# Kernel optimization log

Measured on AMD Instinct MI355X. Metric: run time of the kernel, lower is better.

Reference implementation:

```python
import jax, jax.numpy as jnp
import numpy as np

B, S, HID = 1, 2048, 2048
H, NOPE, ROPE, VDIM = 16, 128, 64, 128
QR, KVR = 1536, 512
IH, ID = 16, 128
TOPK = 512
THETA = 10000.0
EPS = 1e-6
SCALE = (NOPE + ROPE) ** -0.5
NEG = -1e9


def _cos_sin(s, dim, dtype):
    inv = 1.0 / (THETA ** (np.arange(0, dim, 2, dtype=np.float32) / dim))
    t = np.arange(s, dtype=np.float32)
    f = np.outer(t, inv)
    emb = np.concatenate([f, f], -1)
    return jnp.asarray(np.cos(emb), dtype), jnp.asarray(np.sin(emb), dtype)


def _rope(x, cos, sin):
    # x: [b,s,h,d]; cos/sin: [s,d]; NeoX-style rotate_half
    x1, x2 = jnp.split(x, 2, axis=-1)
    rot = jnp.concatenate([-x2, x1], axis=-1)
    return x * cos[None, :, None, :] + rot * sin[None, :, None, :]


def _rmsnorm(x, w):
    v = jnp.mean(x.astype(jnp.float32) ** 2, -1, keepdims=True)
    return (x.astype(jnp.float32) * jax.lax.rsqrt(v + EPS)).astype(x.dtype) * w


def _layernorm(x, w, b):
    m = jnp.mean(x, -1, keepdims=True)
    v = jnp.var(x, -1, keepdims=True)
    return (x - m) * jax.lax.rsqrt(v + EPS) * w + b


def setup_inputs() -> dict:
    key = jax.random.key(0)
    ks = jax.random.split(key, 12)
    g = lambda k, shp: jax.random.normal(k, shp, jnp.float32) * 0.02
    return {
        'hidden_states': jax.random.normal(ks[0], (B, S, HID), jnp.float32),
        'q_a_w': g(ks[1], (QR, HID)),
        'q_a_ln_w': jnp.ones((QR,), jnp.float32),
        'q_b_w': g(ks[2], (H * (NOPE + ROPE), QR)),
        'kv_a_w': g(ks[3], (KVR + ROPE, HID)),
        'kv_a_ln_w': jnp.ones((KVR,), jnp.float32),
        'kv_b_w': g(ks[4], (H * (NOPE + VDIM), KVR)),
        'o_w': g(ks[5], (HID, H * VDIM)),
        'idx_wq_b_w': g(ks[6], (IH * ID, QR)),
        'idx_wk_w': g(ks[7], (ID, HID)),
        'idx_kn_w': jnp.ones((ID,), jnp.float32),
        'idx_kn_b': jnp.zeros((ID,), jnp.float32),
        'idx_wproj_w': g(ks[8], (IH, HID)),
    }


def reference(hidden_states, q_a_w, q_a_ln_w, q_b_w, kv_a_w, kv_a_ln_w, kv_b_w, o_w,
              idx_wq_b_w, idx_wk_w, idx_kn_w, idx_kn_b, idx_wproj_w):
    b, s, _ = hidden_states.shape
    cos, sin = _cos_sin(s, ROPE, hidden_states.dtype)

    # --- MLA projections ---
    qr = _rmsnorm(hidden_states @ q_a_w.T, q_a_ln_w)                 # [b,s,QR]
    q = (qr @ q_b_w.T).reshape(b, s, H, NOPE + ROPE)
    q_nope, q_pe = q[..., :NOPE], q[..., NOPE:]
    q_pe = _rope(q_pe, cos, sin)
    ckv = hidden_states @ kv_a_w.T                                   # [b,s,KVR+ROPE]
    c_kv, k_pe = ckv[..., :KVR], ckv[..., KVR:]
    k_pe = _rope(k_pe[:, :, None, :], cos, sin)                      # [b,s,1,ROPE]
    kv = (_rmsnorm(c_kv, kv_a_ln_w) @ kv_b_w.T).reshape(b, s, H, NOPE + VDIM)
    k_nope, v = kv[..., :NOPE], kv[..., NOPE:]

    # --- DSA indexer: per-token importance scores ---
    iq = (qr @ idx_wq_b_w.T).reshape(b, s, IH, ID)
    iq = jnp.concatenate([_rope(iq[..., :ROPE], cos, sin), iq[..., ROPE:]], -1)
    ik = _layernorm(hidden_states @ idx_wk_w.T, idx_kn_w, idx_kn_b)  # [b,s,ID]
    ik_pe = _rope(ik[:, :, None, :ROPE], cos, sin)[:, :, 0, :]
    ik = jnp.concatenate([ik_pe, ik[..., ROPE:]], -1)
    iw = (hidden_states @ idx_wproj_w.T) * (IH ** -0.5)              # [b,s,IH]
    idx_scores = jnp.einsum('bqh,bhqk->bqk', iw,
                            jax.nn.relu(jnp.einsum('bqhd,bkd->bhqk', iq, ik)))
    causal = jnp.tril(jnp.ones((s, s), bool))
    idx_scores = jnp.where(causal[None], idx_scores, -jnp.inf)
    _, top_idx = jax.lax.top_k(idx_scores, TOPK)                     # [b,s,TOPK]
    bi = jnp.arange(b)[:, None, None]
    qi = jnp.arange(s)[None, :, None]
    keep = jnp.zeros((b, s, s), bool).at[bi, qi, top_idx].set(True)
    allowed = keep & causal[None]                                    # [b,s,s]

    # --- sparse top-k attention (top-k mask to -inf before softmax) ---
    qh = jnp.concatenate([q_nope, q_pe], -1)                         # [b,s,H,192]
    kh = jnp.concatenate([k_nope, jnp.broadcast_to(k_pe, (b, s, H, ROPE))], -1)
    scores = jnp.einsum('bqhd,bkhd->bhqk', qh, kh) * SCALE
    scores = jnp.where(allowed[:, None], scores, NEG)
    attn = jax.nn.softmax(scores, -1)
    out = jnp.einsum('bhqk,bkhd->bqhd', attn, v).reshape(b, s, H * VDIM)
    return out @ o_w.T
```

## Files before the change

### kernel.cpp

```cpp
#include <hip/hip_runtime.h>
#include <hip/hip_bf16.h>
#include <math.h>

#define SEQ 2048
#define HIDD 2048
#define QRANK 1536
#define KVRANK 512
#define TOPK 512
#define EPSF 1e-6f
#define SCALE_ATTN 0.07216878364870323f
#define NCAT 1680

typedef __attribute__((ext_vector_type(8))) short short8v;
typedef __attribute__((ext_vector_type(4))) short short4v;
typedef __attribute__((ext_vector_type(4))) float f32x4;

__device__ inline unsigned short f2bf(float f) {
    unsigned u = __float_as_uint(f);
    unsigned r = (u + 0x7FFFu + ((u >> 16) & 1u)) >> 16;
    return (unsigned short)r;
}
__device__ inline float bf2f(unsigned short b) {
    return __uint_as_float(((unsigned)b) << 16);
}
__device__ inline void split2(float x, unsigned short& h, unsigned short& l) {
    h = f2bf(x);
    l = f2bf(x - bf2f(h));
}

__device__ inline short4v ds_read_tr16(const void* p) {
#if __has_builtin(__builtin_amdgcn_ds_read_tr16_b64)
    return __builtin_amdgcn_ds_read_tr16_b64((short4v*)p);
#else
    const unsigned short* u = (const unsigned short*)p;
    short4v r;
    r[0] = (short)u[0]; r[1] = (short)u[16]; r[2] = (short)u[32]; r[3] = (short)u[48];
    return r;
#endif
}

__global__ void rope_table_kernel(float* __restrict__ cos_t, float* __restrict__ sin_t) {
    int s = blockIdx.x;
    int i = threadIdx.x;
    double inv = pow(10000.0, -((double)(2 * i)) / 64.0);
    double f = (double)s * inv;
    cos_t[s * 32 + i] = (float)cos(f);
    sin_t[s * 32 + i] = (float)sin(f);
}

__global__ __launch_bounds__(256) void cvt_bf16_kernel(const float* __restrict__ in,
                                                       unsigned short* __restrict__ out, int n4) {
    for (int i = blockIdx.x * 256 + threadIdx.x; i < n4; i += gridDim.x * 256) {
        float4 v = ((const float4*)in)[i];
        ushort4 o;
        o.x = f2bf(v.x); o.y = f2bf(v.y); o.z = f2bf(v.z); o.w = f2bf(v.w);
        ((ushort4*)out)[i] = o;
    }
}

__global__ __launch_bounds__(256) void wkt_kernel(const float* __restrict__ kvb,
                                                  unsigned short* __restrict__ wkt) {
    __shared__ float t[128][129];
    int h = blockIdx.x, n0 = blockIdx.y * 128;
    int tid = threadIdx.x;
    for (int it = tid; it < 128 * 32; it += 256) {
        int d = it >> 5, c4 = it & 31;
        float4 v = *(const float4*)(kvb + ((size_t)(h * 256 + d)) * 512 + n0 + c4 * 4);
        t[d][c4 * 4 + 0] = v.x; t[d][c4 * 4 + 1] = v.y;
        t[d][c4 * 4 + 2] = v.z; t[d][c4 * 4 + 3] = v.w;
    }
    __syncthreads();
    for (int it = tid; it < 128 * 32; it += 256) {
        int n = it >> 5, dc = it & 31;
        ushort4 o;
        o.x = f2bf(t[dc * 4 + 0][n]); o.y = f2bf(t[dc * 4 + 1][n]);
        o.z = f2bf(t[dc * 4 + 2][n]); o.w = f2bf(t[dc * 4 + 3][n]);
        *(ushort4*)(wkt + ((size_t)h * 512 + n0 + n) * 128 + dc * 4) = o;
    }
}

__global__ __launch_bounds__(256) void gemm_cat_split_kernel(
    const float* __restrict__ hidden, const float* __restrict__ q_a_w,
    const float* __restrict__ idx_wk_w, const float* __restrict__ idx_wproj_w,
    float* __restrict__ ccat)
{
    __shared__ __align__(16) unsigned short Ah[128 * 32], Al[128 * 32];
    __shared__ __align__(16) unsigned short Bh[128 * 32], Bl[128 * 32];
    int tid = threadIdx.x;
    int l = tid & 63, w = tid >> 6;
    int wr = w >> 1, wc = w & 1;
    int m0 = blockIdx.x * 128, n0 = blockIdx.y * 128;
    f32x4 acc[4][4] = {};
    for (int k0 = 0; k0 < HIDD; k0 += 32) {
        __syncthreads();
#pragma unroll
        for (int i = 0; i < 2; ++i) {
            int idx = tid + i * 256;
            int r = idx >> 2, cc = idx & 3;
            int sw = cc ^ (r & 3);
            {
                const float* src = hidden + (size_t)(m0 + r) * HIDD + k0 + cc * 8;
                float4 f0 = *(const float4*)src, f1 = *(const float4*)(src + 4);
                float xs[8] = {f0.x, f0.y, f0.z, f0.w, f1.x, f1.y, f1.z, f1.w};
                short8v dh, dl;
#pragma unroll
                for (int e = 0; e < 8; ++e) {
                    unsigned short hh, ll; split2(xs[e], hh, ll);
                    dh[e] = (short)hh; dl[e] = (short)ll;
                }
                *(short8v*)&Ah[r * 32 + sw * 8] = dh;
                *(short8v*)&Al[r * 32 + sw * 8] = dl;
            }
            {
                int gb = n0 + r; if (gb > NCAT - 1) gb = NCAT - 1;
                float scale = 1.f;
                const float* src;
                if (gb < 1536) src = q_a_w + (size_t)gb * HIDD;
                else if (gb < 1664) src = idx_wk_w + (size_t)(gb - 1536) * HIDD;
                else { src = idx_wproj_w + (size_t)(gb - 1664) * HIDD; scale = 0.25f; }
                src += k0 + cc * 8;
                float4 f0 = *(const float4*)src, f1 = *(const float4*)(src + 4);
                float xs[8] = {f0.x, f0.y, f0.z, f0.w, f1.x, f1.y, f1.z, f1.w};
                short8v dh, dl;
#pragma unroll
                for (int e = 0; e < 8; ++e) {
                    unsigned short hh, ll; split2(xs[e] * scale, hh, ll);
                    dh[e] = (short)hh; dl[e] = (short)ll;
                }
                *(short8v*)&Bh[r * 32 + sw * 8] = dh;
                *(short8v*)&Bl[r * 32 + sw * 8] = dl;
            }
        }
        __syncthreads();
        short8v avh[4], avl[4];
#pragma unroll
        for (int mt = 0; mt < 4; ++mt) {
            int row = wr * 64 + mt * 16 + (l & 15);
            int ch = (l >> 4) ^ (row & 3);
            avh[mt] = *(const short8v*)&Ah[row * 32 + ch * 8];
            avl[mt] = *(const short8v*)&Al[row * 32 + ch * 8];
        }
#pragma unroll
        for (int nt = 0; nt < 4; ++nt) {
            int row = wc * 64 + nt * 16 + (l & 15);
            int ch = (l >> 4) ^ (row & 3);
            short8v bvh = *(const short8v*)&Bh[row * 32 + ch * 8];
            short8v bvl = *(const short8v*)&Bl[row * 32 + ch * 8];
#pragma unroll
            for (int mt = 0; mt < 4; ++mt) {
                acc[mt][nt] = __builtin_amdgcn_mfma_f32_16x16x32_bf16(avh[mt], bvh, acc[mt][nt], 0, 0, 0);
                acc[mt][nt] = __builtin_amdgcn_mfma_f32_16x16x32_bf16(avh[mt], bvl, acc[mt][nt], 0, 0, 0);
                acc[mt][nt] = __builtin_amdgcn_mfma_f32_16x16x32_bf16(avl[mt], bvh, acc[mt][nt], 0, 0, 0);
            }
        }
    }
#pragma unroll
    for (int mt = 0; mt < 4; ++mt)
#pragma unroll
        for (int nt = 0; nt < 4; ++nt)
#pragma unroll
            for (int i = 0; i < 4; ++i) {
                int gm = m0 + wr * 64 + mt * 16 + (l >> 4) * 4 + i;
                int gn = n0 + wc * 64 + nt * 16 + (l & 15);
                if (gn < NCAT) ccat[(size_t)gm * NCAT + gn] = acc[mt][nt][i];
            }
}

__global__ __launch_bounds__(256) void gemm_iq_split_kernel(
    const float* __restrict__ qr, const float* __restrict__ wq,
    const float* __restrict__ cos_t, const float* __restrict__ sin_t,
    unsigned short* __restrict__ iqh, unsigned short* __restrict__ iql)
{
    __shared__ __align__(16) unsigned short Ah[128 * 32], Al[128 * 32];
    __shared__ __align__(16) unsigned short Bh[128 * 32], Bl[128 * 32];
    int tid = threadIdx.x;
    int l = tid & 63, w = tid >> 6;
    int wr = w >> 1, wc = w & 1;
    int m0 = blockIdx.x * 128, n0 = blockIdx.y * 128;
    int hh_ = blockIdx.y;
    f32x4 acc[4][4] = {};
    for (int k0 = 0; k0 < QRANK; k0 += 32) {
        __syncthreads();
#pragma unroll
        for (int i = 0; i < 2; ++i) {
            int idx = tid + i * 256;
            int r = idx >> 2, cc = idx & 3;
            int sw = cc ^ (r & 3);
            {
                const float* src = qr + (size_t)(m0 + r) * QRANK + k0 + cc * 8;
                float4 f0 = *(const float4*)src, f1 = *(const float4*)(src + 4);
                float xs[8] = {f0.x, f0.y, f0.z, f0.w, f1.x, f1.y, f1.z, f1.w};
                short8v dh, dl;
#pragma unroll
                for (int e = 0; e < 8; ++e) {
                    unsigned short h2, l2; split2(xs[e], h2, l2);
                    dh[e] = (short)h2; dl[e] = (short)l2;
                }
                *(short8v*)&Ah[r * 32 + sw * 8] = dh;
                *(short8v*)&Al[r * 32 + sw * 8] = dl;
            }
            {
                const float* src = wq + (size_t)(n0 + r) * QRANK + k0 + cc * 8;
                float4 f0 = *(const float4*)src, f1 = *(const float4*)(src + 4);
                float xs[8] = {f0.x, f0.y, f0.z, f0.w, f1.x, f1.y, f1.z, f1.w};
                short8v dh, dl;
#pragma unroll
                for (int e = 0; e < 8; ++e) {
                    unsigned short h2, l2; split2(xs[e], h2, l2);
                    dh[e] = (short)h2; dl[e] = (short)l2;
                }
                *(short8v*)&Bh[r * 32 + sw * 8] = dh;
                *(short8v*)&Bl[r * 32 + sw * 8] = dl;
            }
        }
        __syncthreads();
        short8v avh[4], avl[4];
#pragma unroll
        for (int mt = 0; mt < 4; ++mt) {
            int row = wr * 64 + mt * 16 + (l & 15);
            int ch = (l >> 4) ^ (row & 3);
            avh[mt] = *(const short8v*)&Ah[row * 32 + ch * 8];
            avl[mt] = *(const short8v*)&Al[row * 32 + ch * 8];
        }
#pragma unroll
        for (int nt = 0; nt < 4; ++nt) {
            int row = wc * 64 + nt * 16 + (l & 15);
            int ch = (l >> 4) ^ (row & 3);
            short8v bvh = *(const short8v*)&Bh[row * 32 + ch * 8];
            short8v bvl = *(const short8v*)&Bl[row * 32 + ch * 8];
#pragma unroll
            for (int mt = 0; mt < 4; ++mt) {
                acc[mt][nt] = __builtin_amdgcn_mfma_f32_16x16x32_bf16(avh[mt], bvh, acc[mt][nt], 0, 0, 0);
                acc[mt][nt] = __builtin_amdgcn_mfma_f32_16x16x32_bf16(avh[mt], bvl, acc[mt][nt], 0, 0, 0);
                acc[mt][nt] = __builtin_amdgcn_mfma_f32_16x16x32_bf16(avl[mt], bvh, acc[mt][nt], 0, 0, 0);
            }
        }
    }
    if (wc == 0) {
#pragma unroll
        for (int mt = 0; mt < 4; ++mt)
#pragma unroll
            for (int nt = 0; nt < 2; ++nt)
#pragma unroll
                for (int i = 0; i < 4; ++i) {
                    int q = m0 + wr * 64 + mt * 16 + (l >> 4) * 4 + i;
                    int dd = nt * 16 + (l & 15);
                    float c = cos_t[q * 32 + dd], s = sin_t[q * 32 + dd];
                    float x1 = acc[mt][nt][i], x2 = acc[mt][nt + 2][i];
                    acc[mt][nt][i] = x1 * c - x2 * s;
                    acc[mt][nt + 2][i] = x2 * c + x1 * s;
                }
    }
#pragma unroll
    for (int mt = 0; mt < 4; ++mt)
#pragma unroll
        for (int nt = 0; nt < 4; ++nt)
#pragma unroll
            for (int i = 0; i < 4; ++i) {
                int q = m0 + wr * 64 + mt * 16 + (l >> 4) * 4 + i;
                int d = wc * 64 + nt * 16 + (l & 15);
                size_t idx = ((size_t)q * 16 + hh_) * 128 + d;
                unsigned short h2, l2; split2(acc[mt][nt][i], h2, l2);
                iqh[idx] = h2; iql[idx] = l2;
            }
}

template <typename TA, typename TC>
__global__ __launch_bounds__(256) void mfma_nt_kernel(
    const TA* __restrict__ A, const unsigned short* __restrict__ B, TC* __restrict__ C,
    int M, int N, int K, int lda, int ldb, int ldc, long ab, long bb, long cb,
    const float* __restrict__ cos_t, const float* __restrict__ sin_t, int rope_mode)
{
    __shared__ __align__(16) unsigned short Asl[128 * 32];
    __shared__ __align__(16) unsigned short Bsl[128 * 32];
    int z = blockIdx.z;
    const TA* Az = A + (size_t)z * ab;
    const unsigned short* Bz = B + (size_t)z * bb;
    TC* Cz = C + (size_t)z * cb;
    int tid = threadIdx.x;
    int l = tid & 63, w = tid >> 6;
    int wr = w >> 1, wc = w & 1;
    int m0 = blockIdx.x * 128, n0 = blockIdx.y * 128;
    f32x4 acc[4][4] = {};

    for (int k0 = 0; k0 < K; k0 += 32) {
        __syncthreads();
#pragma unroll
        for (int i = 0; i < 2; ++i) {
            int idx = tid + i * 256;
            int r = idx >> 2, cc = idx & 3;
            int sw = cc ^ (r & 3);
            {
                short8v d;
                const TA* src = Az + (size_t)(m0 + r) * lda + k0 + cc * 8;
                if constexpr (sizeof(TA) == 2) {
                    d = *(const short8v*)src;
                } else {
                    float4 f0 = *(const float4*)src;
                    float4 f1 = *(const float4*)(src + 4);
                    d[0] = (short)f2bf(f0.x); d[1] = (short)f2bf(f0.y);
                    d[2] = (short)f2bf(f0.z); d[3] = (short)f2bf(f0.w);
                    d[4] = (short)f2bf(f1.x); d[5] = (short)f2bf(f1.y);
                    d[6] = (short)f2bf(f1.z); d[7] = (short)f2bf(f1.w);
                }
                *(short8v*)&Asl[r * 32 + sw * 8] = d;
            }
            {
                int gb = n0 + r; if (gb > N - 1) gb = N - 1;
                short8v d = *(const short8v*)(Bz + (size_t)gb * ldb + k0 + cc * 8);
                *(short8v*)&Bsl[r * 32 + sw * 8] = d;
            }
        }
        __syncthreads();
        short8v av[4], bv[4];
#pragma unroll
        for (int mt = 0; mt < 4; ++mt) {
            int row = wr * 64 + mt * 16 + (l & 15);
            int ch = (l >> 4) ^ (row & 3);
            av[mt] = *(const short8v*)&Asl[row * 32 + ch * 8];
        }
#pragma unroll
        for (int nt = 0; nt < 4; ++nt) {
            int row = wc * 64 + nt * 16 + (l & 15);
            int ch = (l >> 4) ^ (row & 3);
            bv[nt] = *(const short8v*)&Bsl[row * 32 + ch * 8];
        }
#pragma unroll
        for (int mt = 0; mt < 4; ++mt)
#pragma unroll
            for (int nt = 0; nt < 4; ++nt)
                acc[mt][nt] = __builtin_amdgcn_mfma_f32_16x16x32_bf16(av[mt], bv[nt], acc[mt][nt], 0, 0, 0);
    }
    if (rope_mode) {
        int gcol64 = (n0 >> 6) + wc;
        bool dorope = (rope_mode == 1) ? ((gcol64 % 3) == 2) : (gcol64 == 8);
        if (dorope) {
#pragma unroll
            for (int mt = 0; mt < 4; ++mt)
#pragma unroll
                for (int nt = 0; nt < 2; ++nt)
#pragma unroll
                    for (int i = 0; i < 4; ++i) {
                        int q = m0 + wr * 64 + mt * 16 + (l >> 4) * 4 + i;
                        int dd = nt * 16 + (l & 15);
                        float c = cos_t[q * 32 + dd], sn = sin_t[q * 32 + dd];
                        float x1 = acc[mt][nt][i], x2 = acc[mt][nt + 2][i];
                        acc[mt][nt][i] = x1 * c - x2 * sn;
                        acc[mt][nt + 2][i] = x2 * c + x1 * sn;
                    }
        }
    }
#pragma unroll
    for (int mt = 0; mt < 4; ++mt) {
#pragma unroll
        for (int nt = 0; nt < 4; ++nt) {
#pragma unroll
            for (int i = 0; i < 4; ++i) {
                int gm = m0 + wr * 64 + mt * 16 + (l >> 4) * 4 + i;
                int gn = n0 + wc * 64 + nt * 16 + (l & 15);
                if (gn < N) {
                    float v = acc[mt][nt][i];
                    if constexpr (sizeof(TC) == 4) Cz[(size_t)gm * ldc + gn] = v;
                    else Cz[(size_t)gm * ldc + gn] = f2bf(v);
                }
            }
        }
    }
}

__global__ __launch_bounds__(256) void rmsnorm_kernel(
    const float* __restrict__ in, const float* __restrict__ w, float* __restrict__ out,
    unsigned short* __restrict__ bf_out, int n, int in_stride)
{
    int row = blockIdx.x, tid = threadIdx.x;
    const float* x = in + (size_t)row * in_stride;
    float4 v[2];
    int cnt = 0;
    float ss = 0.f;
    int nf4 = n >> 2;
    for (int i = tid; i < nf4; i += 256) {
        float4 t = *(const float4*)(x + i * 4);
        v[cnt++] = t;
        ss += t.x * t.x + t.y * t.y + t.z * t.z + t.w * t.w;
    }
#pragma unroll
    for (int m = 32; m; m >>= 1) ss += __shfl_xor(ss, m);
    __shared__ float red[8];
    int wid = tid >> 6;
    if ((tid & 63) == 0) red[wid] = ss;
    __syncthreads();
    if (tid == 0) {
        float s = red[0] + red[1] + red[2] + red[3];
        red[4] = rsqrtf(s / (float)n + EPSF);
    }
    __syncthreads();
    float scale = red[4];
    cnt = 0;
    for (int i = tid; i < nf4; i += 256) {
        float4 t = v[cnt++];
        float4 wv = *(const float4*)(w + i * 4);
        float4 o;
        o.x = t.x * scale * wv.x; o.y = t.y * scale * wv.y;
        o.z = t.z * scale * wv.z; o.w = t.w * scale * wv.w;
        *(float4*)(out + (size_t)row * n + i * 4) = o;
        if (bf_out) {
            ushort4 ob;
            ob.x = f2bf(o.x); ob.y = f2bf(o.y); ob.z = f2bf(o.z); ob.w = f2bf(o.w);
            *(ushort4*)(bf_out + (size_t)row * n + i * 4) = ob;
        }
    }
}

__global__ __launch_bounds__(256) void rmsnorm_khg_kernel(
    const float* __restrict__ ckv, const float* __restrict__ w,
    unsigned short* __restrict__ khg)
{
    int row = blockIdx.x, tid = threadIdx.x;
    const float* x = ckv + (size_t)row * 576;
    float4 v = make_float4(0.f, 0.f, 0.f, 0.f);
    float ss = 0.f;
    if (tid < 128) {
        v = *(const float4*)(x + tid * 4);
        ss = v.x * v.x + v.y * v.y + v.z * v.z + v.w * v.w;
    }
#pragma unroll
    for (int mm = 32; mm; mm >>= 1) ss += __shfl_xor(ss, mm);
    __shared__ float red[8];
    if ((tid & 63) == 0) red[tid >> 6] = ss;
    __syncthreads();
    if (tid == 0) red[4] = rsqrtf((red[0] + red[1] + red[2] + red[3]) * (1.f / 512.f) + EPSF);
    __syncthreads();
    float scale = red[4];
    if (tid < 128) {
        float4 wv = *(const float4*)(w + tid * 4);
        ushort4 ob;
        ob.x = f2bf(v.x * scale * wv.x); ob.y = f2bf(v.y * scale * wv.y);
        ob.z = f2bf(v.z * scale * wv.z); ob.w = f2bf(v.w * scale * wv.w);
        *(ushort4*)(khg + (size_t)row * 576 + tid * 4) = ob;
    } else if (tid < 192) {
        khg[(size_t)row * 576 + 512 + (tid - 128)] = f2bf(x[512 + tid - 128]);
    }
}

__global__ __launch_bounds__(64) void ln_rope_split_kernel(
    const float* __restrict__ in, int stride,
    const float* __restrict__ w, const float* __restrict__ b,
    const float* __restrict__ cos_t, const float* __restrict__ sin_t,
    unsigned short* __restrict__ ikh, unsigned short* __restrict__ ikl)
{
    int row = blockIdx.x, tid = threadIdx.x;
    const float* x = in + (size_t)row * stride;
    float x0 = x[tid], x1 = x[tid + 64];
    float s = x0 + x1, ss = x0 * x0 + x1 * x1;
#pragma unroll
    for (int m = 32; m; m >>= 1) { s += __shfl_xor(s, m); ss += __shfl_xor(ss, m); }
    float mean = s * (1.f / 128.f);
    float var = ss * (1.f / 128.f) - mean * mean;
    float r = rsqrtf(var + EPSF);
    float n0 = (x0 - mean) * r * w[tid] + b[tid];
    float n1 = (x1 - mean) * r * w[tid + 64] + b[tid + 64];
    float c = cos_t[row * 32 + (tid & 31)], sn = sin_t[row * 32 + (tid & 31)];
    float other = __shfl_xor(n0, 32);
    float r0 = (tid < 32) ? (n0 * c - other * sn) : (n0 * c + other * sn);
    unsigned short h2, l2;
    split2(r0, h2, l2);
    ikh[(size_t)row * 128 + tid] = h2; ikl[(size_t)row * 128 + tid] = l2;
    split2(n1, h2, l2);
    ikh[(size_t)row * 128 + 64 + tid] = h2; ikl[(size_t)row * 128 + 64 + tid] = l2;
}

__global__ __launch_bounds__(256) void idx_scores_mfma_kernel(
    const unsigned short* __restrict__ iqh, const unsigned short* __restrict__ iql,
    const unsigned short* __restrict__ ikh, const unsigned short* __restrict__ ikl,
    const float* __restrict__ iwsrc, int iw_stride,
    float* __restrict__ scores)
{
    int q0 = blockIdx.x * 64, k0 = blockIdx.y * 64;
    int tid = threadIdx.x;
    if (k0 > q0 + 63) {
        for (int t = tid; t < 64 * 64; t += 256) {
            int r = t >> 6, c = t & 63;
            scores[(size_t)(q0 + r) * SEQ + k0 + c] = -INFINITY;
        }
        return;
    }
    __shared__ __align__(16) unsigned short skh[64 * 128], skl[64 * 128];
    __shared__ __align__(16) unsigned short sqh[64 * 128], sql[64 * 128];
    __shared__ float iws[64][16];
    int l = tid & 63, w = tid >> 6;
    for (int it = tid; it < 64 * 16; it += 256) {
        int r = it >> 4, c = it & 15;
        int sw = c ^ (r & 15);
        *(short8v*)&skh[r * 128 + sw * 8] = *(const short8v*)(ikh + (size_t)(k0 + r) * 128 + c * 8);
        *(short8v*)&skl[r * 128 + sw * 8] = *(const short8v*)(ikl + (size_t)(k0 + r) * 128 + c * 8);
    }
    {
        int r = tid >> 2, c = tid & 3;
        *(float4*)&iws[r][c * 4] = *(const float4*)(iwsrc + (size_t)(q0 + r) * iw_stride + c * 4);
    }
    f32x4 acc[4] = {};
    for (int h = 0; h < 16; ++h) {
        __syncthreads();
        for (int it = tid; it < 64 * 16; it += 256) {
            int r = it >> 4, c = it & 15;
            int sw = c ^ (r & 15);
            size_t base = ((size_t)(q0 + r) * 16 + h) * 128 + c * 8;
            *(short8v*)&sqh[r * 128 + sw * 8] = *(const short8v*)(iqh + base);
            *(short8v*)&sql[r * 128 + sw * 8] = *(const short8v*)(iql + base);
        }
        __syncthreads();
        f32x4 dot[4] = {};
#pragma unroll
        for (int ks = 0; ks < 4; ++ks) {
            int arow = w * 16 + (l & 15);
            int ach = ((l >> 4) + ks * 4) ^ (arow & 15);
            short8v ah = *(const short8v*)&sqh[arow * 128 + ach * 8];
            short8v al = *(const short8v*)&sql[arow * 128 + ach * 8];
#pragma unroll
            for (int nt = 0; nt < 4; ++nt) {
                int brow = nt * 16 + (l & 15);
                int bch = ((l >> 4) + ks * 4) ^ (brow & 15);
                short8v bh = *(const short8v*)&skh[brow * 128 + bch * 8];
                short8v bl = *(const short8v*)&skl[brow * 128 + bch * 8];
                dot[nt] = __builtin_amdgcn_mfma_f32_16x16x32_bf16(ah, bh, dot[nt], 0, 0, 0);
                dot[nt] = __builtin_amdgcn_mfma_f32_16x16x32_bf16(ah, bl, dot[nt], 0, 0, 0);
                dot[nt] = __builtin_amdgcn_mfma_f32_16x16x32_bf16(al, bh, dot[nt], 0, 0, 0);
            }
        }
#pragma unroll
        for (int nt = 0; nt < 4; ++nt)
#pragma unroll
            for (int i = 0; i < 4; ++i) {
                float wv = iws[w * 16 + (l >> 4) * 4 + i][h];
                acc[nt][i] += wv * fmaxf(dot[nt][i], 0.f);
            }
    }
#pragma unroll
    for (int nt = 0; nt < 4; ++nt)
#pragma unroll
        for (int i = 0; i < 4; ++i) {
            int q = q0 + w * 16 + (l >> 4) * 4 + i;
            int k = k0 + nt * 16 + (l & 15);
            scores[(size_t)q * SEQ + k] = (k <= q) ? acc[nt][i] : -INFINITY;
        }
}

__global__ __launch_bounds__(1024) void topk_kernel(
    const float* __restrict__ scores, int* __restrict__ sel)
{
    int qi = blockIdx.x, tid = threadIdx.x;
    __shared__ unsigned long long keys[2048];
    const float* srow = scores + (size_t)qi * SEQ;
#pragma unroll
    for (int r = 0; r < 2; ++r) {
        int k = tid + r * 1024;
        unsigned u = __float_as_uint(srow[k]);
        unsigned mv = (u & 0x80000000u) ? ~u : (u | 0x80000000u);
        keys[k] = ((unsigned long long)mv << 32) | (unsigned)(2047 - k);
    }
    for (int ksz = 2; ksz <= 2048; ksz <<= 1) {
        for (int j = ksz >> 1; j > 0; j >>= 1) {
            __syncthreads();
#pragma unroll 1
            for (int r = 0; r < 2; ++r) {
                int i = tid + r * 1024;
                int ixj = i ^ j;
                if (ixj > i) {
                    unsigned long long a = keys[i], b = keys[ixj];
                    bool dir = ((i & ksz) == 0);
                    if ((a < b) == dir) { keys[i] = b; keys[ixj] = a; }
                }
            }
        }
    }
    __syncthreads();
    if (tid < TOPK) {
        int k = 2047 - (int)(keys[tid] & 0xFFFFFFFFu);
        sel[(size_t)qi * TOPK + tid] = (tid <= qi) ? k : -1;
    }
}

__global__ __launch_bounds__(256) void attn_mfma_kernel(
    const unsigned short* __restrict__ qabs,
    const float* __restrict__ qsrc,
    const unsigned short* __restrict__ khg,
    const int* __restrict__ sel,
    unsigned short* __restrict__ ocomp)
{
    __shared__ __align__(16) char smem[39424];
    unsigned short* plds = (unsigned short*)(smem + 38016);
    float* smax = (float*)(smem + 39040);
    float* ssum = (float*)(smem + 39168);
    int* selb   = (int*)(smem + 39296);

    const int qi = blockIdx.x;
    const int tid = threadIdx.x;
    const int l = tid & 63, w = tid >> 6;
    const int lg = l >> 4, lr = l & 15;
    const int nv = min(TOPK, qi + 1);
    const int ntile = (nv + 31) >> 5;
    const int krow = w * 16 + lr;

    short8v aq[18];
    {
        const unsigned short* qa = qabs + ((size_t)qi * 16 + lr) * 512 + lg * 8;
#pragma unroll
        for (int ks = 0; ks < 16; ++ks)
            aq[ks] = *(const short8v*)(qa + ks * 32);
        const float* qp = qsrc + (size_t)qi * 3072 + lr * 192 + 128 + lg * 8;
#pragma unroll
        for (int ks = 0; ks < 2; ++ks) {
            float4 f0 = *(const float4*)(qp + ks * 32);
            float4 f1 = *(const float4*)(qp + ks * 32 + 4);
            short8v d;
            d[0] = (short)f2bf(f0.x); d[1] = (short)f2bf(f0.y);
            d[2] = (short)f2bf(f0.z); d[3] = (short)f2bf(f0.w);
            d[4] = (short)f2bf(f1.x); d[5] = (short)f2bf(f1.y);
            d[6] = (short)f2bf(f1.z); d[7] = (short)f2bf(f1.w);
            aq[16 + ks] = d;
        }
    }

    const int sbase = krow * 32 + (lg >> 1) * 1056 + (lg & 1) * 16;
    const int vboff = w * 8 * 1056 + lg * 256 + lr * 2;

    float m[4] = {-1e30f, -1e30f, -1e30f, -1e30f};
    float lsum[4] = {0.f, 0.f, 0.f, 0.f};
    f32x4 oacc[8] = {};

    for (int t = 0; t < ntile; ++t) {
        const int j0 = t * 32;
        __syncthreads();
        if (tid < 32) {
            int sv = sel[(size_t)qi * TOPK + j0 + tid];
            selb[tid] = sv < 0 ? 0 : sv;
        }
        __syncthreads();
        for (int it = tid; it < 32 * 64; it += 256) {
            int key = it >> 6, c = it & 63;
            short8v v = *(const short8v*)(khg + (size_t)selb[key] * 576 + c * 8);
            *(short8v*)(smem + (c >> 1) * 1056 + key * 32 + (c & 1) * 16) = v;
        }
        {
            int key = tid >> 3, c = tid & 7;
            short8v v = *(const short8v*)(khg + (size_t)selb[key] * 576 + 512 + c * 8);
            *(short8v*)(smem + (32 + (c >> 1)) * 1056 + key * 32 + (c & 1) * 16) = v;
        }
        __syncthreads();
        f32x4 s = {};
        if (w < 2) {
            __builtin_amdgcn_s_setprio(1);
#pragma unroll
            for (int ks = 0; ks < 18; ++ks) {
                short8v b = *(const short8v*)(smem + sbase + ks * 2112);
                s = __builtin_amdgcn_mfma_f32_16x16x32_bf16(aq[ks], b, s, 0, 0, 0);
            }
            __builtin_amdgcn_s_setprio(0);
            bool kvalid = (j0 + krow) < nv;
#pragma unroll
            for (int i = 0; i < 4; ++i)
                s[i] = kvalid ? s[i] * SCALE_ATTN : -1e30f;
            float tm[4];
#pragma unroll
            for (int i = 0; i < 4; ++i) tm[i] = s[i];
#pragma unroll
            for (int sh = 1; sh < 16; sh <<= 1)
#pragma unroll
                for (int i = 0; i < 4; ++i) tm[i] = fmaxf(tm[i], __shfl_xor(tm[i], sh));
            if (lr == 0) *(float4*)&smax[w * 16 + lg * 4] = make_float4(tm[0], tm[1], tm[2], tm[3]);
        }
        __syncthreads();
        float mn[4], scl[4];
#pragma unroll
        for (int i = 0; i < 4; ++i) {
            int h = lg * 4 + i;
            float tmax = fmaxf(smax[h], smax[16 + h]);
            mn[i] = fmaxf(m[i], tmax);
            scl[i] = __expf(m[i] - mn[i]);
            m[i] = mn[i];
        }
        if (w < 2) {
            float p[4], rs[4];
#pragma unroll
            for (int i = 0; i < 4; ++i) { p[i] = __expf(s[i] - mn[i]); rs[i] = p[i]; }
#pragma unroll
            for (int sh = 1; sh < 16; sh <<= 1)
#pragma unroll
                for (int i = 0; i < 4; ++i) rs[i] += __shfl_xor(rs[i], sh);
            if (lr == 0) *(float4*)&ssum[w * 16 + lg * 4] = make_float4(rs[0], rs[1], rs[2], rs[3]);
            ushort4 pb;
            pb.x = f2bf(p[0]); pb.y = f2bf(p[1]); pb.z = f2bf(p[2]); pb.w = f2bf(p[3]);
            *(ushort4*)&plds[krow * 16 + lg * 4] = pb;
        }
        __syncthreads();
#pragma unroll
        for (int i = 0; i < 4; ++i) {
            int h = lg * 4 + i;
            lsum[i] = lsum[i] * scl[i] + (ssum[h] + ssum[16 + h]);
        }
#pragma unroll
        for (int nt = 0; nt < 8; ++nt)
#pragma unroll
            for (int i = 0; i < 4; ++i) oacc[nt][i] *= scl[i];
        short8v af;
#pragma unroll
        for (int j = 0; j < 8; ++j)
            af[j] = (short)plds[(lg * 8 + j) * 16 + lr];
        __builtin_amdgcn_s_setprio(1);
#pragma unroll
        for (int nt = 0; nt < 8; ++nt) {
            const char* a = smem + vboff + nt * 1056;
            short4v t0 = ds_read_tr16(a);
            short4v t1 = ds_read_tr16(a + 128);
            short8v bf = __builtin_shufflevector(t0, t1, 0, 1, 2, 3, 4, 5, 6, 7);
            oacc[nt] = __builtin_amdgcn_mfma_f32_16x16x32_bf16(af, bf, oacc[nt], 0, 0, 0);
        }
        __builtin_amdgcn_s_setprio(0);
    }
    float inv[4];
#pragma unroll
    for (int i = 0; i < 4; ++i) inv[i] = 1.f / lsum[i];
    unsigned short* ob = ocomp + (size_t)qi * 16 * 512;
#pragma unroll
    for (int nt = 0; nt < 8; ++nt) {
        int d = w * 128 + nt * 16 + lr;
#pragma unroll
        for (int i = 0; i < 4; ++i) {
            int h = lg * 4 + i;
            ob[h * 512 + d] = f2bf(oacc[nt][i] * inv[i]);
        }
    }
}

extern "C" void kernel_launch(void* const* d_in, const int* in_sizes, int n_in,
                              void* d_out, int out_size, void* d_ws, size_t ws_size,
                              hipStream_t stream) {
    (void)in_sizes; (void)n_in; (void)out_size; (void)ws_size;
    const float* hidden      = (const float*)d_in[0];
    const float* q_a_w       = (const float*)d_in[1];
    const float* q_a_ln_w    = (const float*)d_in[2];
    const float* q_b_w       = (const float*)d_in[3];
    const float* kv_a_w      = (const float*)d_in[4];
    const float* kv_a_ln_w   = (const float*)d_in[5];
    const float* kv_b_w      = (const float*)d_in[6];
    const float* o_w         = (const float*)d_in[7];
    const float* idx_wq_b_w  = (const float*)d_in[8];
    const float* idx_wk_w    = (const float*)d_in[9];
    const float* idx_kn_w    = (const float*)d_in[10];
    const float* idx_kn_b    = (const float*)d_in[11];
    const float* idx_wproj_w = (const float*)d_in[12];
    float* out = (float*)d_out;

    char* ws = (char*)d_ws;
    size_t off = 0;
    auto alloc = [&](size_t nbytes) -> void* {
        void* p = ws + off;
        off = (off + nbytes + 255) & ~(size_t)255;
        return p;
    };
    float* cos_t = (float*)alloc((size_t)SEQ * 32 * 4);
    float* sin_t = (float*)alloc((size_t)SEQ * 32 * 4);
    float* qbuf  = (float*)alloc((size_t)SEQ * 3072 * 4);
    float* ckv   = (float*)alloc((size_t)SEQ * 576 * 4);
    int*   sel   = (int*)alloc((size_t)SEQ * TOPK * 4);
    unsigned short* khg      = (unsigned short*)alloc((size_t)SEQ * 576 * 2);
    unsigned short* attno_bf = (unsigned short*)alloc((size_t)SEQ * 2048 * 2);
    unsigned short* qr_bf    = (unsigned short*)alloc((size_t)SEQ * QRANK * 2);
    unsigned short* q_b_bf   = (unsigned short*)alloc((size_t)3072 * QRANK * 2);
    unsigned short* kv_a_bf  = (unsigned short*)alloc((size_t)576 * HIDD * 2);
    unsigned short* o_w_bf   = (unsigned short*)alloc((size_t)HIDD * 2048 * 2);
    unsigned short* kv_b_bf  = (unsigned short*)alloc((size_t)4096 * 512 * 2);
    unsigned short* wkt      = (unsigned short*)alloc((size_t)16 * 512 * 128 * 2);
    size_t mark = off;
    float* qr    = (float*)alloc((size_t)SEQ * QRANK * 4);
    float* ccat  = (float*)alloc((size_t)SEQ * NCAT * 4);
    float* scores = (float*)alloc((size_t)SEQ * SEQ * 4);
    unsigned short* iqh = (unsigned short*)alloc((size_t)SEQ * 2048 * 2);
    unsigned short* iql = (unsigned short*)alloc((size_t)SEQ * 2048 * 2);
    unsigned short* ikh = (unsigned short*)alloc((size_t)SEQ * 128 * 2);
    unsigned short* ikl = (unsigned short*)alloc((size_t)SEQ * 128 * 2);
    off = mark;
    unsigned short* qabsb = (unsigned short*)alloc((size_t)SEQ * 16 * 512 * 2);
    unsigned short* ocomp = (unsigned short*)alloc((size_t)SEQ * 16 * 512 * 2);

    rope_table_kernel<<<dim3(SEQ), dim3(32), 0, stream>>>(cos_t, sin_t);

    cvt_bf16_kernel<<<1024, 256, 0, stream>>>(q_b_w, q_b_bf, 3072 * QRANK / 4);
    cvt_bf16_kernel<<<1024, 256, 0, stream>>>(kv_a_w, kv_a_bf, 576 * HIDD / 4);
    cvt_bf16_kernel<<<1024, 256, 0, stream>>>(o_w, o_w_bf, HIDD * 2048 / 4);
    cvt_bf16_kernel<<<1024, 256, 0, stream>>>(kv_b_w, kv_b_bf, 4096 * 512 / 4);
    wkt_kernel<<<dim3(16, 4), 256, 0, stream>>>(kv_b_w, wkt);

    gemm_cat_split_kernel<<<dim3(16, 14), 256, 0, stream>>>(hidden, q_a_w, idx_wk_w, idx_wproj_w, ccat);

    rmsnorm_kernel<<<SEQ, 256, 0, stream>>>(ccat, q_a_ln_w, qr, qr_bf, QRANK, NCAT);

    ln_rope_split_kernel<<<SEQ, 64, 0, stream>>>(ccat + 1536, NCAT, idx_kn_w, idx_kn_b, cos_t, sin_t, ikh, ikl);

    mfma_nt_kernel<unsigned short, float><<<dim3(16, 24, 1), 256, 0, stream>>>(
        qr_bf, q_b_bf, qbuf, SEQ, 3072, QRANK, QRANK, QRANK, 3072, 0L, 0L, 0L,
        cos_t, sin_t, 1);

    mfma_nt_kernel<float, float><<<dim3(16, 5, 1), 256, 0, stream>>>(
        hidden, kv_a_bf, ckv, SEQ, 576, HIDD, HIDD, HIDD, 576, 0L, 0L, 0L,
        cos_t, sin_t, 2);
    rmsnorm_khg_kernel<<<SEQ, 256, 0, stream>>>(ckv, kv_a_ln_w, khg);

    gemm_iq_split_kernel<<<dim3(16, 16), 256, 0, stream>>>(qr, idx_wq_b_w, cos_t, sin_t, iqh, iql);

    idx_scores_mfma_kernel<<<dim3(32, 32), 256, 0, stream>>>(iqh, iql, ikh, ikl, ccat + 1664, NCAT, scores);
    topk_kernel<<<SEQ, 1024, 0, stream>>>(scores, sel);

    mfma_nt_kernel<float, unsigned short><<<dim3(16, 4, 16), 256, 0, stream>>>(
        qbuf, wkt, qabsb, SEQ, 512, 128, 3072, 128, 16 * 512,
        192L, 512L * 128L, 512L, nullptr, nullptr, 0);

    attn_mfma_kernel<<<SEQ, 256, 0, stream>>>(qabsb, qbuf, khg, sel, ocomp);

    mfma_nt_kernel<unsigned short, unsigned short><<<dim3(16, 1, 16), 256, 0, stream>>>(
        ocomp, kv_b_bf + (size_t)128 * 512, attno_bf, SEQ, 128, 512,
        16 * 512, 512, 2048, 512L, 256L * 512L, 128L, nullptr, nullptr, 0);

    mfma_nt_kernel<unsigned short, float><<<dim3(16, 16, 1), 256, 0, stream>>>(
        attno_bf, o_w_bf, out, SEQ, HIDD, 2048, 2048, 2048, HIDD, 0L, 0L, 0L,
        nullptr, nullptr, 0);
}
```

Baseline: 960.0 us.

## Widen attention key tiles to 64, hoist indexer K fragments, merge bf16 conversions

The sparse attention kernel now processes 64 selected keys per tile instead of 32, so all four waves compute scores rather than two. The rope part of K moves to a separate XOR-swizzled LDS region, and PV runs as two k-blocks. LDS use roughly doubles, which may lower occupancy. The indexer score kernel loads the K high/low fragments into registers once instead of reloading them from LDS for every head, at the cost of many more VGPRs. The four weight-conversion launches are merged into one kernel to cut launch overhead.

```diff
diff --git a/kernel.cpp b/kernel.cpp
--- a/kernel.cpp
+++ b/kernel.cpp
@@ -48,13 +48,23 @@
     sin_t[s * 32 + i] = (float)sin(f);
 }
 
-__global__ __launch_bounds__(256) void cvt_bf16_kernel(const float* __restrict__ in,
-                                                       unsigned short* __restrict__ out, int n4) {
-    for (int i = blockIdx.x * 256 + threadIdx.x; i < n4; i += gridDim.x * 256) {
-        float4 v = ((const float4*)in)[i];
+__global__ __launch_bounds__(256) void cvt_bf16_4_kernel(
+    const float* __restrict__ a, int na4, const float* __restrict__ b, int nb4,
+    const float* __restrict__ c, int nc4, const float* __restrict__ d, int nd4,
+    unsigned short* __restrict__ oa, unsigned short* __restrict__ ob,
+    unsigned short* __restrict__ oc, unsigned short* __restrict__ od)
+{
+    int total = na4 + nb4 + nc4 + nd4;
+    for (int i = blockIdx.x * 256 + threadIdx.x; i < total; i += gridDim.x * 256) {
+        const float* src; unsigned short* dst; int j = i;
+        if (j < na4) { src = a; dst = oa; }
+        else if ((j -= na4) < nb4) { src = b; dst = ob; }
+        else if ((j -= nb4) < nc4) { src = c; dst = oc; }
+        else { j -= nc4; src = d; dst = od; }
+        float4 v = ((const float4*)src)[j];
         ushort4 o;
         o.x = f2bf(v.x); o.y = f2bf(v.y); o.z = f2bf(v.z); o.w = f2bf(v.w);
-        ((ushort4*)out)[i] = o;
+        ((ushort4*)dst)[j] = o;
     }
 }
 
@@ -498,6 +508,17 @@
         int r = tid >> 2, c = tid & 3;
         *(float4*)&iws[r][c * 4] = *(const float4*)(iwsrc + (size_t)(q0 + r) * iw_stride + c * 4);
     }
+    __syncthreads();
+    short8v bhr[4][4], blr[4][4];
+#pragma unroll
+    for (int nt = 0; nt < 4; ++nt)
+#pragma unroll
+        for (int ks = 0; ks < 4; ++ks) {
+            int brow = nt * 16 + (l & 15);
+            int bch = ((l >> 4) + ks * 4) ^ (brow & 15);
+            bhr[nt][ks] = *(const short8v*)&skh[brow * 128 + bch * 8];
+            blr[nt][ks] = *(const short8v*)&skl[brow * 128 + bch * 8];
+        }
     f32x4 acc[4] = {};
     for (int h = 0; h < 16; ++h) {
         __syncthreads();
@@ -518,13 +539,9 @@
             short8v al = *(const short8v*)&sql[arow * 128 + ach * 8];
 #pragma unroll
             for (int nt = 0; nt < 4; ++nt) {
-                int brow = nt * 16 + (l & 15);
-                int bch = ((l >> 4) + ks * 4) ^ (brow & 15);
-                short8v bh = *(const short8v*)&skh[brow * 128 + bch * 8];
-                short8v bl = *(const short8v*)&skl[brow * 128 + bch * 8];
-                dot[nt] = __builtin_amdgcn_mfma_f32_16x16x32_bf16(ah, bh, dot[nt], 0, 0, 0);
-                dot[nt] = __builtin_amdgcn_mfma_f32_16x16x32_bf16(ah, bl, dot[nt], 0, 0, 0);
-                dot[nt] = __builtin_amdgcn_mfma_f32_16x16x32_bf16(al, bh, dot[nt], 0, 0, 0);
+                dot[nt] = __builtin_amdgcn_mfma_f32_16x16x32_bf16(ah, bhr[nt][ks], dot[nt], 0, 0, 0);
+                dot[nt] = __builtin_amdgcn_mfma_f32_16x16x32_bf16(ah, blr[nt][ks], dot[nt], 0, 0, 0);
+                dot[nt] = __builtin_amdgcn_mfma_f32_16x16x32_bf16(al, bhr[nt][ks], dot[nt], 0, 0, 0);
             }
         }
 #pragma unroll
@@ -587,18 +604,18 @@
     const int* __restrict__ sel,
     unsigned short* __restrict__ ocomp)
 {
-    __shared__ __align__(16) char smem[39424];
-    unsigned short* plds = (unsigned short*)(smem + 38016);
-    float* smax = (float*)(smem + 39040);
-    float* ssum = (float*)(smem + 39168);
-    int* selb   = (int*)(smem + 39296);
+    __shared__ __align__(16) char smem[77568];
+    unsigned short* plds = (unsigned short*)(smem + 74752);
+    float* smax = (float*)(smem + 76800);
+    float* ssum = (float*)(smem + 77056);
+    int* selb   = (int*)(smem + 77312);
 
     const int qi = blockIdx.x;
     const int tid = threadIdx.x;
     const int l = tid & 63, w = tid >> 6;
     const int lg = l >> 4, lr = l & 15;
     const int nv = min(TOPK, qi + 1);
-    const int ntile = (nv + 31) >> 5;
+    const int ntile = (nv + 63) >> 6;
     const int krow = w * 16 + lr;
 
     short8v aq[18];
@@ -621,101 +638,105 @@
         }
     }
 
-    const int sbase = krow * 32 + (lg >> 1) * 1056 + (lg & 1) * 16;
-    const int vboff = w * 8 * 1056 + lg * 256 + lr * 2;
+    const int sbase = krow * 32 + (lg >> 1) * 2080 + (lg & 1) * 16;
+    const int vboff = w * 16640 + lg * 256 + lr * 2;
 
     float m[4] = {-1e30f, -1e30f, -1e30f, -1e30f};
     float lsum[4] = {0.f, 0.f, 0.f, 0.f};
     f32x4 oacc[8] = {};
 
     for (int t = 0; t < ntile; ++t) {
-        const int j0 = t * 32;
-        __syncthreads();
-        if (tid < 32) {
+        const int j0 = t * 64;
+        __syncthreads();
+        if (tid < 64) {
             int sv = sel[(size_t)qi * TOPK + j0 + tid];
             selb[tid] = sv < 0 ? 0 : sv;
         }
         __syncthreads();
-        for (int it = tid; it < 32 * 64; it += 256) {
+        for (int it = tid; it < 64 * 64; it += 256) {
             int key = it >> 6, c = it & 63;
             short8v v = *(const short8v*)(khg + (size_t)selb[key] * 576 + c * 8);
-            *(short8v*)(smem + (c >> 1) * 1056 + key * 32 + (c & 1) * 16) = v;
-        }
-        {
-            int key = tid >> 3, c = tid & 7;
+            *(short8v*)(smem + (c >> 1) * 2080 + key * 32 + (c & 1) * 16) = v;
+        }
+        for (int it = tid; it < 64 * 8; it += 256) {
+            int key = it >> 3, c = it & 7;
             short8v v = *(const short8v*)(khg + (size_t)selb[key] * 576 + 512 + c * 8);
-            *(short8v*)(smem + (32 + (c >> 1)) * 1056 + key * 32 + (c & 1) * 16) = v;
+            *(short8v*)(smem + 66560 + ((key * 128 + c * 16) ^ ((key & 7) << 4))) = v;
         }
         __syncthreads();
         f32x4 s = {};
-        if (w < 2) {
-            __builtin_amdgcn_s_setprio(1);
-#pragma unroll
-            for (int ks = 0; ks < 18; ++ks) {
-                short8v b = *(const short8v*)(smem + sbase + ks * 2112);
-                s = __builtin_amdgcn_mfma_f32_16x16x32_bf16(aq[ks], b, s, 0, 0, 0);
-            }
-            __builtin_amdgcn_s_setprio(0);
-            bool kvalid = (j0 + krow) < nv;
-#pragma unroll
-            for (int i = 0; i < 4; ++i)
-                s[i] = kvalid ? s[i] * SCALE_ATTN : -1e30f;
-            float tm[4];
-#pragma unroll
-            for (int i = 0; i < 4; ++i) tm[i] = s[i];
-#pragma unroll
-            for (int sh = 1; sh < 16; sh <<= 1)
-#pragma unroll
-                for (int i = 0; i < 4; ++i) tm[i] = fmaxf(tm[i], __shfl_xor(tm[i], sh));
-            if (lr == 0) *(float4*)&smax[w * 16 + lg * 4] = make_float4(tm[0], tm[1], tm[2], tm[3]);
-        }
+#pragma unroll
+        for (int ks = 0; ks < 16; ++ks) {
+            short8v b = *(const short8v*)(smem + sbase + ks * 4160);
+            s = __builtin_amdgcn_mfma_f32_16x16x32_bf16(aq[ks], b, s, 0, 0, 0);
+        }
+#pragma unroll
+        for (int ks = 0; ks < 2; ++ks) {
+            short8v b = *(const short8v*)(smem + 66560 +
+                ((krow * 128 + ks * 64 + lg * 16) ^ ((krow & 7) << 4)));
+            s = __builtin_amdgcn_mfma_f32_16x16x32_bf16(aq[16 + ks], b, s, 0, 0, 0);
+        }
+        bool kvalid = (j0 + krow) < nv;
+#pragma unroll
+        for (int i = 0; i < 4; ++i)
+            s[i] = kvalid ? s[i] * SCALE_ATTN : -1e30f;
+        float tm[4];
+#pragma unroll
+        for (int i = 0; i < 4; ++i) tm[i] = s[i];
+#pragma unroll
+        for (int sh = 1; sh < 16; sh <<= 1)
+#pragma unroll
+            for (int i = 0; i < 4; ++i) tm[i] = fmaxf(tm[i], __shfl_xor(tm[i], sh));
+        if (lr == 0) *(float4*)&smax[w * 16 + lg * 4] = make_float4(tm[0], tm[1], tm[2], tm[3]);
         __syncthreads();
         float mn[4], scl[4];
 #pragma unroll
         for (int i = 0; i < 4; ++i) {
             int h = lg * 4 + i;
-            float tmax = fmaxf(smax[h], smax[16 + h]);
+            float tmax = fmaxf(fmaxf(smax[h], smax[16 + h]), fmaxf(smax[32 + h], smax[48 + h]));
             mn[i] = fmaxf(m[i], tmax);
             scl[i] = __expf(m[i] - mn[i]);
             m[i] = mn[i];
         }
-        if (w < 2) {
-            float p[4], rs[4];
-#pragma unroll
-            for (int i = 0; i < 4; ++i) { p[i] = __expf(s[i] - mn[i]); rs[i] = p[i]; }
-#pragma unroll
-            for (int sh = 1; sh < 16; sh <<= 1)
-#pragma unroll
-                for (int i = 0; i < 4; ++i) rs[i] += __shfl_xor(rs[i], sh);
-            if (lr == 0) *(float4*)&ssum[w * 16 + lg * 4] = make_float4(rs[0], rs[1], rs[2], rs[3]);
+        float p[4], rs[4];
+#pragma unroll
+        for (int i = 0; i < 4; ++i) { p[i] = __expf(s[i] - mn[i]); rs[i] = p[i]; }
+#pragma unroll
+        for (int sh = 1; sh < 16; sh <<= 1)
+#pragma unroll
+            for (int i = 0; i < 4; ++i) rs[i] += __shfl_xor(rs[i], sh);
+        if (lr == 0) *(float4*)&ssum[w * 16 + lg * 4] = make_float4(rs[0], rs[1], rs[2], rs[3]);
+        {
             ushort4 pb;
             pb.x = f2bf(p[0]); pb.y = f2bf(p[1]); pb.z = f2bf(p[2]); pb.w = f2bf(p[3]);
-            *(ushort4*)&plds[krow * 16 + lg * 4] = pb;
+            *(ushort4*)&plds[(w * 16 + lr) * 16 + lg * 4] = pb;
         }
         __syncthreads();
 #pragma unroll
         for (int i = 0; i < 4; ++i) {
             int h = lg * 4 + i;
-            lsum[i] = lsum[i] * scl[i] + (ssum[h] + ssum[16 + h]);
+            float ts = ssum[h] + ssum[16 + h] + ssum[32 + h] + ssum[48 + h];
+            lsum[i] = lsum[i] * scl[i] + ts;
         }
 #pragma unroll
         for (int nt = 0; nt < 8; ++nt)
 #pragma unroll
             for (int i = 0; i < 4; ++i) oacc[nt][i] *= scl[i];
-        short8v af;
-#pragma unroll
-        for (int j = 0; j < 8; ++j)
-            af[j] = (short)plds[(lg * 8 + j) * 16 + lr];
-        __builtin_amdgcn_s_setprio(1);
-#pragma unroll
-        for (int nt = 0; nt < 8; ++nt) {
-            const char* a = smem + vboff + nt * 1056;
-            short4v t0 = ds_read_tr16(a);
-            short4v t1 = ds_read_tr16(a + 128);
-            short8v bf = __builtin_shufflevector(t0, t1, 0, 1, 2, 3, 4, 5, 6, 7);
-            oacc[nt] = __builtin_amdgcn_mfma_f32_16x16x32_bf16(af, bf, oacc[nt], 0, 0, 0);
-        }
-        __builtin_amdgcn_s_setprio(0);
+#pragma unroll
+        for (int kb = 0; kb < 2; ++kb) {
+            short8v af;
+#pragma unroll
+            for (int j = 0; j < 8; ++j)
+                af[j] = (short)plds[(kb * 32 + lg * 8 + j) * 16 + lr];
+#pragma unroll
+            for (int nt = 0; nt < 8; ++nt) {
+                const char* a = smem + vboff + kb * 1024 + nt * 2080;
+                short4v t0 = ds_read_tr16(a);
+                short4v t1 = ds_read_tr16(a + 128);
+                short8v bf = __builtin_shufflevector(t0, t1, 0, 1, 2, 3, 4, 5, 6, 7);
+                oacc[nt] = __builtin_amdgcn_mfma_f32_16x16x32_bf16(af, bf, oacc[nt], 0, 0, 0);
+            }
+        }
     }
     float inv[4];
 #pragma unroll
@@ -785,10 +806,10 @@
 
     rope_table_kernel<<<dim3(SEQ), dim3(32), 0, stream>>>(cos_t, sin_t);
 
-    cvt_bf16_kernel<<<1024, 256, 0, stream>>>(q_b_w, q_b_bf, 3072 * QRANK / 4);
-    cvt_bf16_kernel<<<1024, 256, 0, stream>>>(kv_a_w, kv_a_bf, 576 * HIDD / 4);
-    cvt_bf16_kernel<<<1024, 256, 0, stream>>>(o_w, o_w_bf, HIDD * 2048 / 4);
-    cvt_bf16_kernel<<<1024, 256, 0, stream>>>(kv_b_w, kv_b_bf, 4096 * 512 / 4);
+    cvt_bf16_4_kernel<<<2048, 256, 0, stream>>>(
+        q_b_w, 3072 * QRANK / 4, kv_a_w, 576 * HIDD / 4,
+        o_w, HIDD * 2048 / 4, kv_b_w, 4096 * 512 / 4,
+        q_b_bf, kv_a_bf, o_w_bf, kv_b_bf);
     wkt_kernel<<<dim3(16, 4), 256, 0, stream>>>(kv_b_w, wkt);
 
     gemm_cat_split_kernel<<<dim3(16, 14), 256, 0, stream>>>(hidden, q_a_w, idx_wk_w, idx_wproj_w, ccat);
```

Result: faster. 882.8 us (-8.0%).
